# Kernel optimization log

Hardware: AMD Instinct MI355X
Metric: run time of the kernel (lower is better)

Reference implementation:

```python
import jax, jax.numpy as jnp
import numpy as np

N_NODES = 100000
N_EDGES = 3200000
D_FEAT = 128
HIDDEN = 16
N_CLASSES = 7


def gcn_conv(x, edge_index, edge_weight, W, b, n_nodes):
    h = x @ W  # dense projection first (Fout small)
    src, dst = edge_index[0], edge_index[1]
    # add self-loops with weight 1
    loop = jnp.arange(n_nodes, dtype=edge_index.dtype)
    src_a = jnp.concatenate([src, loop])
    dst_a = jnp.concatenate([dst, loop])
    ew_a = jnp.concatenate([edge_weight, jnp.ones((n_nodes,), dtype=x.dtype)])
    deg = jax.ops.segment_sum(ew_a, dst_a, num_segments=n_nodes)
    dinv = jnp.where(deg > 0, jax.lax.rsqrt(deg), 0.0)
    norm = dinv[src_a] * ew_a * dinv[dst_a]  # [E+N]
    msg = h[src_a] * norm[:, None]  # gather + scale
    out = jax.ops.segment_sum(msg, dst_a, num_segments=n_nodes)
    return out + b


def setup_inputs() -> dict:
    key = jax.random.key(0)
    k = jax.random.split(key, 8)
    x = jax.random.normal(k[0], (N_NODES, D_FEAT), dtype=jnp.float32)
    edge_index = jax.random.randint(k[1], (2, N_EDGES), 0, N_NODES, dtype=jnp.int64)
    edge_weight = jax.random.uniform(k[2], (N_EDGES,), dtype=jnp.float32)
    s1 = 1.0 / np.sqrt(D_FEAT)
    s2 = 1.0 / np.sqrt(HIDDEN)
    W1 = jax.random.uniform(k[3], (D_FEAT, HIDDEN), jnp.float32, -s1, s1)
    b1 = jnp.zeros((HIDDEN,), jnp.float32)
    W2 = jax.random.uniform(k[4], (HIDDEN, N_CLASSES), jnp.float32, -s2, s2)
    b2 = jnp.zeros((N_CLASSES,), jnp.float32)
    return {"x": x, "edge_index": edge_index, "edge_weight": edge_weight,
            "W1": W1, "b1": b1, "W2": W2, "b2": b2}


def reference(x, edge_index, edge_weight, W1, b1, W2, b2):
    h = jax.nn.relu(gcn_conv(x, edge_index, edge_weight, W1, b1, N_NODES))
    out = gcn_conv(h, edge_index, edge_weight, W2, b2, N_NODES)
    return jax.nn.log_softmax(out, axis=1)
```

## Files before the change

### kernel.cpp

```cpp
#include <hip/hip_runtime.h>
#include <hip/hip_fp16.h>
#include <math.h>

constexpr int NN = 100000;
constexpr int NE = 3200000;
constexpr int DF = 128;
constexpr int NH = 16;
constexpr int NC = 7;

constexpr int BN    = 256;
constexpr int NB    = (NN + BN - 1) / BN;
constexpr int CAP   = 9216;
constexpr int CHUNK = 4096;
constexpr int AB    = (NE + CHUNK - 1) / CHUNK;
constexpr int EPT   = CHUNK / 1024;
constexpr int SPT   = (CAP + 1023) / 1024;

constexpr float QS   = 32767.0f;
constexpr float QINV = 1.0f / 32767.0f;

typedef _Float16 half8 __attribute__((ext_vector_type(8)));
typedef float    f32x4 __attribute__((ext_vector_type(4)));

__global__ void k_zero(int* __restrict__ gcur) {
    int t = blockIdx.x * blockDim.x + threadIdx.x;
    if (t < NB) gcur[t] = 0;
}

__global__ void __launch_bounds__(1024)
k_append(const int* __restrict__ src,
         const int* __restrict__ dst,
         const float* __restrict__ w,
         int* __restrict__ gcur,
         uint2* __restrict__ ebuf) {
    __shared__ int hist[NB];
    __shared__ int cscan[512];
    __shared__ int basev[NB];
    __shared__ uint2 staged[CHUNK];
    __shared__ unsigned short sbkt[CHUNK];
    for (int i = threadIdx.x; i < NB; i += 1024) hist[i] = 0;
    __syncthreads();
    int e0 = blockIdx.x * CHUNK;
    unsigned slo[EPT], sw[EPT];
    int sbr[EPT];
#pragma unroll
    for (int k = 0; k < EPT; ++k) {
        int e = e0 + (int)threadIdx.x + k * 1024;
        sbr[k] = -1;
        if (e < NE) {
            int d = __builtin_nontemporal_load(dst + e);
            int b = d >> 8;
            int r = atomicAdd(&hist[b], 1);
            slo[k] = ((unsigned)(d & (BN - 1)) << 17) |
                     (unsigned)__builtin_nontemporal_load(src + e);
            sw[k]  = (unsigned)(__builtin_nontemporal_load(w + e) * QS + 0.5f);
            sbr[k] = (b << 13) | r;
        }
    }
    __syncthreads();
    {
        int v0 = (threadIdx.x < NB) ? hist[threadIdx.x] : 0;
        if (threadIdx.x < 512) cscan[threadIdx.x] = v0;
        __syncthreads();
        for (int off = 1; off < 512; off <<= 1) {
            int v = (threadIdx.x < 512 && threadIdx.x >= off) ? cscan[threadIdx.x - off] : 0;
            __syncthreads();
            if (threadIdx.x < 512) cscan[threadIdx.x] += v;
            __syncthreads();
        }
    }
    if (threadIdx.x < NB) {
        int c = hist[threadIdx.x];
        basev[threadIdx.x] = (c > 0) ? atomicAdd(&gcur[threadIdx.x], c) : 0;
    }
    __syncthreads();
#pragma unroll
    for (int k = 0; k < EPT; ++k) {
        if (sbr[k] >= 0) {
            int b = sbr[k] >> 13;
            int idx = (cscan[b] - hist[b]) + (sbr[k] & 0x1FFF);
            uint2 v; v.x = slo[k]; v.y = sw[k];
            staged[idx] = v;
            sbkt[idx] = (unsigned short)b;
        }
    }
    __syncthreads();
    int total = min(CHUNK, NE - e0);
    for (int i = threadIdx.x; i < total; i += 1024) {
        int b = sbkt[i];
        int st = cscan[b] - hist[b];
        int pos = basev[b] + (i - st);
        if (pos < CAP) ebuf[(size_t)b * CAP + pos] = staged[i];
    }
}

__global__ void __launch_bounds__(1024)
k_sort(const int* __restrict__ gcur,
       uint2* __restrict__ ebuf,
       int* __restrict__ rs,
       int* __restrict__ rc,
       float* __restrict__ dinv) {
    __shared__ int cursor[BN];
    __shared__ int scanS[BN];
    __shared__ int startEx[BN];
    __shared__ unsigned sorted[CAP];
    int b = blockIdx.x;
    int tid = threadIdx.x;
    int cnt = min(gcur[b], CAP);
    const uint2* eb = ebuf + (size_t)b * CAP;
    if (tid < BN) cursor[tid] = 0;
    __syncthreads();
    unsigned sval[SPT];
    int sdr[SPT];
#pragma unroll
    for (int k = 0; k < SPT; ++k) {
        int i = tid + k * 1024;
        sdr[k] = -1;
        if (i < cnt) {
            uint2 v = eb[i];
            int dl = (v.x >> 17) & (BN - 1);
            int r = atomicAdd(&cursor[dl], 1);
            sval[k] = (v.x & 0x1FFFF) | (v.y << 17);
            sdr[k] = (dl << 14) | r;
        }
    }
    __syncthreads();
    if (tid < BN) scanS[tid] = cursor[tid];
    __syncthreads();
    for (int off = 1; off < BN; off <<= 1) {
        int v = (tid < BN && tid >= off) ? scanS[tid - off] : 0;
        __syncthreads();
        if (tid < BN) scanS[tid] += v;
        __syncthreads();
    }
    if (tid < BN) {
        int ex = scanS[tid] - cursor[tid];
        startEx[tid] = ex;
        int n = b * BN + tid;
        if (n < NN) { rs[n] = b * CAP * 2 + ex; rc[n] = cursor[tid]; }
    }
    __syncthreads();
#pragma unroll
    for (int k = 0; k < SPT; ++k) {
        if (sdr[k] >= 0)
            sorted[startEx[sdr[k] >> 14] + (sdr[k] & 0x3FFF)] = sval[k];
    }
    __syncthreads();
    unsigned* eb32 = (unsigned*)ebuf + (size_t)b * CAP * 2;
    for (int i = tid; i < cnt; i += 1024) eb32[i] = sorted[i];
    {
        int node = tid >> 2, part = tid & 3;
        float s = (part == 0) ? 1.0f : 0.0f;
        int s0 = startEx[node], c = cursor[node];
        for (int i = part; i < c; i += 4) s += (float)(sorted[s0 + i] >> 17) * QINV;
        s += __shfl_xor(s, 1, 4);
        s += __shfl_xor(s, 2, 4);
        if (part == 0) {
            int n = b * BN + node;
            if (n < NN) dinv[n] = rsqrtf(s);
        }
    }
}

__global__ void __launch_bounds__(256)
k_proj1(const float* __restrict__ x,
        const float* __restrict__ W1,
        const float* __restrict__ dinv,
        __half* __restrict__ h1p) {
    int wave = threadIdx.x >> 6;
    int lane = threadIdx.x & 63;
    int tile = blockIdx.x * 4 + wave;
    if (tile * 16 >= NN) return;
    int m    = lane & 15;
    int quad = lane >> 4;
    half8 bfrag[4];
#pragma unroll
    for (int kc = 0; kc < 4; ++kc)
#pragma unroll
        for (int j = 0; j < 8; ++j)
            bfrag[kc][j] = (_Float16)W1[(kc * 32 + quad * 8 + j) * NH + m];
    int base = tile * 16;
    const float* xr = x + (size_t)(base + m) * DF + quad * 8;
    f32x4 acc = {0.f, 0.f, 0.f, 0.f};
#pragma unroll
    for (int kc = 0; kc < 4; ++kc) {
        const float4* p = (const float4*)(xr + kc * 32);
        float4 u0 = p[0];
        float4 u1 = p[1];
        half8 afrag;
        afrag[0] = (_Float16)u0.x; afrag[1] = (_Float16)u0.y;
        afrag[2] = (_Float16)u0.z; afrag[3] = (_Float16)u0.w;
        afrag[4] = (_Float16)u1.x; afrag[5] = (_Float16)u1.y;
        afrag[6] = (_Float16)u1.z; afrag[7] = (_Float16)u1.w;
        acc = __builtin_amdgcn_mfma_f32_16x16x32_f16(afrag, bfrag[kc], acc, 0, 0, 0);
    }
    float4 d4 = *(const float4*)(dinv + base + quad * 4);
#pragma unroll
    for (int reg = 0; reg < 4; ++reg) {
        float dd = (reg == 0) ? d4.x : (reg == 1) ? d4.y : (reg == 2) ? d4.z : d4.w;
        int row = quad * 4 + reg;
        h1p[(size_t)(base + row) * 16 + m] = __float2half(acc[reg] * dd);
    }
}

__global__ void __launch_bounds__(256)
k_agg1p(const int* __restrict__ rs,
        const int* __restrict__ rc,
        const unsigned* __restrict__ cbuf,
        const __half* __restrict__ h1p,
        const float* __restrict__ dinv,
        const float* __restrict__ b1,
        const float* __restrict__ W2,
        __half* __restrict__ h2p) {
    const uint2* hp4 = (const uint2*)h1p;
    int t = blockIdx.x * 256 + threadIdx.x;
    int n = t >> 2;
    int f4 = t & 3;
    if (n >= NN) return;
    float a0, a1, a2, a3;
    {
        uint2 u = hp4[n * 4 + f4];
        float2 lo = __half22float2(*(const __half2*)&u.x);
        float2 hi = __half22float2(*(const __half2*)&u.y);
        a0 = lo.x; a1 = lo.y; a2 = hi.x; a3 = hi.y;
    }
    int s0 = rs[n], c = rc[n];
    for (int i = 0; i < c; i += 8) {
        unsigned e[8];
        uint2 u[8];
#pragma unroll
        for (int k = 0; k < 8; ++k) {
            int idx = i + k;
            e[k] = (idx < c) ? __builtin_nontemporal_load(cbuf + s0 + idx) : 0u;
        }
#pragma unroll
        for (int k = 0; k < 8; ++k)
            u[k] = hp4[(e[k] & 0x1FFFF) * 4 + f4];
#pragma unroll
        for (int k = 0; k < 8; ++k) {
            float w = (float)(e[k] >> 17) * QINV;
            float2 lo = __half22float2(*(const __half2*)&u[k].x);
            float2 hi = __half22float2(*(const __half2*)&u[k].y);
            a0 += w * lo.x; a1 += w * lo.y; a2 += w * hi.x; a3 += w * hi.y;
        }
    }
    float di = dinv[n];
    int fb = 4 * f4;
    float hr0 = fmaxf(di * a0 + b1[fb + 0], 0.0f);
    float hr1 = fmaxf(di * a1 + b1[fb + 1], 0.0f);
    float hr2 = fmaxf(di * a2 + b1[fb + 2], 0.0f);
    float hr3 = fmaxf(di * a3 + b1[fb + 3], 0.0f);
    float p0, p1, p2, p3, p4, p5, p6;
    {
        const float* w0r = W2 + (fb + 0) * NC;
        const float* w1r = W2 + (fb + 1) * NC;
        const float* w2r = W2 + (fb + 2) * NC;
        const float* w3r = W2 + (fb + 3) * NC;
        p0 = hr0 * w0r[0] + hr1 * w1r[0] + hr2 * w2r[0] + hr3 * w3r[0];
        p1 = hr0 * w0r[1] + hr1 * w1r[1] + hr2 * w2r[1] + hr3 * w3r[1];
        p2 = hr0 * w0r[2] + hr1 * w1r[2] + hr2 * w2r[2] + hr3 * w3r[2];
        p3 = hr0 * w0r[3] + hr1 * w1r[3] + hr2 * w2r[3] + hr3 * w3r[3];
        p4 = hr0 * w0r[4] + hr1 * w1r[4] + hr2 * w2r[4] + hr3 * w3r[4];
        p5 = hr0 * w0r[5] + hr1 * w1r[5] + hr2 * w2r[5] + hr3 * w3r[5];
        p6 = hr0 * w0r[6] + hr1 * w1r[6] + hr2 * w2r[6] + hr3 * w3r[6];
    }
#pragma unroll
    for (int mask = 1; mask < 4; mask <<= 1) {
        p0 += __shfl_xor(p0, mask, 4);
        p1 += __shfl_xor(p1, mask, 4);
        p2 += __shfl_xor(p2, mask, 4);
        p3 += __shfl_xor(p3, mask, 4);
        p4 += __shfl_xor(p4, mask, 4);
        p5 += __shfl_xor(p5, mask, 4);
        p6 += __shfl_xor(p6, mask, 4);
    }
    float pa = (f4 == 0) ? p0 : (f4 == 1) ? p2 : (f4 == 2) ? p4 : p6;
    float pb = (f4 == 0) ? p1 : (f4 == 1) ? p3 : (f4 == 2) ? p5 : 0.0f;
    __half2 hv;
    hv.x = __float2half(di * pa);
    hv.y = __float2half(di * pb);
    ((__half2*)h2p)[n * 4 + f4] = hv;
}

__global__ void __launch_bounds__(256)
k_agg2_lsm(const int* __restrict__ rs,
           const int* __restrict__ rc,
           const unsigned* __restrict__ cbuf,
           const __half* __restrict__ h2p,
           const float* __restrict__ dinv,
           const float* __restrict__ b2,
           float* __restrict__ out) {
    const uint2* hp2 = (const uint2*)h2p;
    int t = blockIdx.x * 256 + threadIdx.x;
    int n = t >> 1;
    int c2 = t & 1;
    if (n >= NN) return;
    float a0, a1, a2, a3;
    {
        uint2 u = hp2[n * 2 + c2];
        float2 lo = __half22float2(*(const __half2*)&u.x);
        float2 hi = __half22float2(*(const __half2*)&u.y);
        a0 = lo.x; a1 = lo.y; a2 = hi.x; a3 = hi.y;
    }
    int s0 = rs[n], c = rc[n];
    for (int i = 0; i < c; i += 8) {
        unsigned e[8];
        uint2 u[8];
#pragma unroll
        for (int k = 0; k < 8; ++k) {
            int idx = i + k;
            e[k] = (idx < c) ? __builtin_nontemporal_load(cbuf + s0 + idx) : 0u;
        }
#pragma unroll
        for (int k = 0; k < 8; ++k)
            u[k] = hp2[(e[k] & 0x1FFFF) * 2 + c2];
#pragma unroll
        for (int k = 0; k < 8; ++k) {
            float w = (float)(e[k] >> 17) * QINV;
            float2 lo = __half22float2(*(const __half2*)&u[k].x);
            float2 hi = __half22float2(*(const __half2*)&u[k].y);
            a0 += w * lo.x; a1 += w * lo.y; a2 += w * hi.x; a3 += w * hi.y;
        }
    }
    float di = dinv[n];
    int cb = 4 * c2;
    float va0 = di * a0 + b2[cb + 0];
    float va1 = di * a1 + b2[cb + 1];
    float va2 = di * a2 + b2[cb + 2];
    float va3 = (c2 == 0) ? (di * a3 + b2[3]) : -1e30f;
    float m = fmaxf(fmaxf(va0, va1), fmaxf(va2, va3));
    m = fmaxf(m, __shfl_xor(m, 1, 2));
    float s = __expf(va0 - m) + __expf(va1 - m) + __expf(va2 - m) + __expf(va3 - m);
    s += __shfl_xor(s, 1, 2);
    float lse = m + __logf(s);
    int base = n * NC + cb;
    out[base + 0] = va0 - lse;
    out[base + 1] = va1 - lse;
    out[base + 2] = va2 - lse;
    if (c2 == 0) out[base + 3] = va3 - lse;
}

extern "C" void kernel_launch(void* const* d_in, const int* in_sizes, int n_in,
                              void* d_out, int out_size, void* d_ws, size_t ws_size,
                              hipStream_t stream) {
    const float* x  = (const float*)d_in[0];
    const int*   ei = (const int*)d_in[1];
    const float* ew = (const float*)d_in[2];
    const float* W1 = (const float*)d_in[3];
    const float* b1 = (const float*)d_in[4];
    const float* W2 = (const float*)d_in[5];
    const float* b2 = (const float*)d_in[6];
    float* out = (float*)d_out;

    const int* srcp = ei;
    const int* dstp = ei + NE;

    float*  ws   = (float*)d_ws;
    float*  dinv = ws;
    __half* h1p  = (__half*)(ws + 100352);
    __half* h2p  = (__half*)(ws + 900352);
    int*    gcur = (int*)(ws + 1300352);
    int*    rs   = (int*)(ws + 1301376);
    int*    rc   = (int*)(ws + 1401728);
    uint2*  ebuf = (uint2*)(ws + 1502080);
    const unsigned* cbuf = (const unsigned*)ebuf;

    auto cdiv = [](long long a, long long b) { return (int)((a + b - 1) / b); };

    k_zero<<<1, 1024, 0, stream>>>(gcur);
    k_append<<<AB, 1024, 0, stream>>>(srcp, dstp, ew, gcur, ebuf);
    k_sort<<<NB, 1024, 0, stream>>>(gcur, ebuf, rs, rc, dinv);
    k_proj1<<<cdiv(NN, 64), 256, 0, stream>>>(x, W1, dinv, h1p);
    k_agg1p<<<cdiv((long long)NN * 4, 256), 256, 0, stream>>>(rs, rc, cbuf, h1p, dinv, b1, W2, h2p);
    k_agg2_lsm<<<cdiv((long long)NN * 2, 256), 256, 0, stream>>>(rs, rc, cbuf, h2p, dinv, b2, out);
}
```

Before: 259.3 us.

## Replace per-node CSR sort with bucket-level aggregation via shared-memory atomics

Removes the per-bucket counting sort that built a CSR layout, and keeps edges only binned by 256-node destination bucket, with a separate byte array for the local destination. Degree and both aggregation layers now run one 1024-thread block per bucket, accumulating into padded shared-memory float arrays with LDS atomics. The append kernel's block scan is rewritten with wave shuffles, and the zero kernel is swapped for a memset. This trades the sort pass and its extra global traffic for heavy shared-atomic contention and per-edge 16-lane atomic fan-out. Float summation order also becomes nondeterministic.

```diff
diff --git a/kernel.cpp b/kernel.cpp
--- a/kernel.cpp
+++ b/kernel.cpp
@@ -14,64 +14,72 @@
 constexpr int CHUNK = 4096;
 constexpr int AB    = (NE + CHUNK - 1) / CHUNK;
 constexpr int EPT   = CHUNK / 1024;
-constexpr int SPT   = (CAP + 1023) / 1024;
 
 constexpr float QS   = 32767.0f;
 constexpr float QINV = 1.0f / 32767.0f;
 
 typedef _Float16 half8 __attribute__((ext_vector_type(8)));
 typedef float    f32x4 __attribute__((ext_vector_type(4)));
-
-__global__ void k_zero(int* __restrict__ gcur) {
-    int t = blockIdx.x * blockDim.x + threadIdx.x;
-    if (t < NB) gcur[t] = 0;
-}
 
 __global__ void __launch_bounds__(1024)
 k_append(const int* __restrict__ src,
          const int* __restrict__ dst,
          const float* __restrict__ w,
          int* __restrict__ gcur,
-         uint2* __restrict__ ebuf) {
+         unsigned* __restrict__ eval,
+         unsigned char* __restrict__ edl) {
     __shared__ int hist[NB];
     __shared__ int cscan[512];
     __shared__ int basev[NB];
-    __shared__ uint2 staged[CHUNK];
-    __shared__ unsigned short sbkt[CHUNK];
-    for (int i = threadIdx.x; i < NB; i += 1024) hist[i] = 0;
+    __shared__ int wsum[8];
+    __shared__ unsigned sval32[CHUNK];
+    __shared__ unsigned smeta[CHUNK];
+    int tid = threadIdx.x;
+    for (int i = tid; i < NB; i += 1024) hist[i] = 0;
     __syncthreads();
     int e0 = blockIdx.x * CHUNK;
-    unsigned slo[EPT], sw[EPT];
+    unsigned sv[EPT], sm[EPT];
     int sbr[EPT];
 #pragma unroll
     for (int k = 0; k < EPT; ++k) {
-        int e = e0 + (int)threadIdx.x + k * 1024;
+        int e = e0 + tid + k * 1024;
         sbr[k] = -1;
         if (e < NE) {
             int d = __builtin_nontemporal_load(dst + e);
             int b = d >> 8;
             int r = atomicAdd(&hist[b], 1);
-            slo[k] = ((unsigned)(d & (BN - 1)) << 17) |
-                     (unsigned)__builtin_nontemporal_load(src + e);
-            sw[k]  = (unsigned)(__builtin_nontemporal_load(w + e) * QS + 0.5f);
+            unsigned q = (unsigned)(__builtin_nontemporal_load(w + e) * QS + 0.5f);
+            sv[k] = (q << 17) |
+                    (unsigned)__builtin_nontemporal_load(src + e);
+            sm[k] = ((unsigned)b << 8) | (unsigned)(d & (BN - 1));
             sbr[k] = (b << 13) | r;
         }
     }
     __syncthreads();
     {
-        int v0 = (threadIdx.x < NB) ? hist[threadIdx.x] : 0;
-        if (threadIdx.x < 512) cscan[threadIdx.x] = v0;
+        int v = 0;
+        if (tid < 512) {
+            v = (tid < NB) ? hist[tid] : 0;
+#pragma unroll
+            for (int d = 1; d < 64; d <<= 1) {
+                int u = __shfl_up(v, d, 64);
+                if ((tid & 63) >= d) v += u;
+            }
+            if ((tid & 63) == 63) wsum[tid >> 6] = v;
+        }
         __syncthreads();
-        for (int off = 1; off < 512; off <<= 1) {
-            int v = (threadIdx.x < 512 && threadIdx.x >= off) ? cscan[threadIdx.x - off] : 0;
-            __syncthreads();
-            if (threadIdx.x < 512) cscan[threadIdx.x] += v;
-            __syncthreads();
-        }
-    }
-    if (threadIdx.x < NB) {
-        int c = hist[threadIdx.x];
-        basev[threadIdx.x] = (c > 0) ? atomicAdd(&gcur[threadIdx.x], c) : 0;
+        if (tid == 0) {
+            int acc = 0;
+#pragma unroll
+            for (int i = 0; i < 8; ++i) { int t = wsum[i]; wsum[i] = acc; acc += t; }
+        }
+        __syncthreads();
+        if (tid < 512) cscan[tid] = v + wsum[tid >> 6];
+    }
+    __syncthreads();
+    if (tid < NB) {
+        int c = hist[tid];
+        basev[tid] = (c > 0) ? atomicAdd(&gcur[tid], c) : 0;
     }
     __syncthreads();
 #pragma unroll
@@ -79,86 +87,46 @@
         if (sbr[k] >= 0) {
             int b = sbr[k] >> 13;
             int idx = (cscan[b] - hist[b]) + (sbr[k] & 0x1FFF);
-            uint2 v; v.x = slo[k]; v.y = sw[k];
-            staged[idx] = v;
-            sbkt[idx] = (unsigned short)b;
+            sval32[idx] = sv[k];
+            smeta[idx]  = sm[k];
         }
     }
     __syncthreads();
     int total = min(CHUNK, NE - e0);
-    for (int i = threadIdx.x; i < total; i += 1024) {
-        int b = sbkt[i];
+    for (int i = tid; i < total; i += 1024) {
+        unsigned mv = smeta[i];
+        int b = (int)(mv >> 8);
         int st = cscan[b] - hist[b];
         int pos = basev[b] + (i - st);
-        if (pos < CAP) ebuf[(size_t)b * CAP + pos] = staged[i];
+        if (pos < CAP) {
+            size_t g = (size_t)b * CAP + pos;
+            eval[g] = sval32[i];
+            edl[g]  = (unsigned char)(mv & 0xFF);
+        }
     }
 }
 
 __global__ void __launch_bounds__(1024)
-k_sort(const int* __restrict__ gcur,
-       uint2* __restrict__ ebuf,
-       int* __restrict__ rs,
-       int* __restrict__ rc,
+k_dinv(const int* __restrict__ gcur,
+       const unsigned* __restrict__ eval,
+       const unsigned char* __restrict__ edl,
        float* __restrict__ dinv) {
-    __shared__ int cursor[BN];
-    __shared__ int scanS[BN];
-    __shared__ int startEx[BN];
-    __shared__ unsigned sorted[CAP];
+    __shared__ float deg[BN];
     int b = blockIdx.x;
     int tid = threadIdx.x;
     int cnt = min(gcur[b], CAP);
-    const uint2* eb = ebuf + (size_t)b * CAP;
-    if (tid < BN) cursor[tid] = 0;
-    __syncthreads();
-    unsigned sval[SPT];
-    int sdr[SPT];
-#pragma unroll
-    for (int k = 0; k < SPT; ++k) {
-        int i = tid + k * 1024;
-        sdr[k] = -1;
-        if (i < cnt) {
-            uint2 v = eb[i];
-            int dl = (v.x >> 17) & (BN - 1);
-            int r = atomicAdd(&cursor[dl], 1);
-            sval[k] = (v.x & 0x1FFFF) | (v.y << 17);
-            sdr[k] = (dl << 14) | r;
-        }
-    }
-    __syncthreads();
-    if (tid < BN) scanS[tid] = cursor[tid];
-    __syncthreads();
-    for (int off = 1; off < BN; off <<= 1) {
-        int v = (tid < BN && tid >= off) ? scanS[tid - off] : 0;
-        __syncthreads();
-        if (tid < BN) scanS[tid] += v;
-        __syncthreads();
-    }
+    const unsigned* ev = eval + (size_t)b * CAP;
+    const unsigned char* ed = edl + (size_t)b * CAP;
+    if (tid < BN) deg[tid] = 1.0f;
+    __syncthreads();
+    for (int i = tid; i < cnt; i += 1024) {
+        float w = (float)(ev[i] >> 17) * QINV;
+        atomicAdd(&deg[ed[i]], w);
+    }
+    __syncthreads();
     if (tid < BN) {
-        int ex = scanS[tid] - cursor[tid];
-        startEx[tid] = ex;
         int n = b * BN + tid;
-        if (n < NN) { rs[n] = b * CAP * 2 + ex; rc[n] = cursor[tid]; }
-    }
-    __syncthreads();
-#pragma unroll
-    for (int k = 0; k < SPT; ++k) {
-        if (sdr[k] >= 0)
-            sorted[startEx[sdr[k] >> 14] + (sdr[k] & 0x3FFF)] = sval[k];
-    }
-    __syncthreads();
-    unsigned* eb32 = (unsigned*)ebuf + (size_t)b * CAP * 2;
-    for (int i = tid; i < cnt; i += 1024) eb32[i] = sorted[i];
-    {
-        int node = tid >> 2, part = tid & 3;
-        float s = (part == 0) ? 1.0f : 0.0f;
-        int s0 = startEx[node], c = cursor[node];
-        for (int i = part; i < c; i += 4) s += (float)(sorted[s0 + i] >> 17) * QINV;
-        s += __shfl_xor(s, 1, 4);
-        s += __shfl_xor(s, 2, 4);
-        if (part == 0) {
-            int n = b * BN + node;
-            if (n < NN) dinv[n] = rsqrtf(s);
-        }
+        if (n < NN) dinv[n] = rsqrtf(deg[tid]);
     }
 }
 
@@ -203,141 +171,158 @@
     }
 }
 
-__global__ void __launch_bounds__(256)
-k_agg1p(const int* __restrict__ rs,
-        const int* __restrict__ rc,
-        const unsigned* __restrict__ cbuf,
+__global__ void __launch_bounds__(1024)
+k_agg1B(const int* __restrict__ gcur,
+        const unsigned* __restrict__ eval,
+        const unsigned char* __restrict__ edl,
         const __half* __restrict__ h1p,
         const float* __restrict__ dinv,
         const float* __restrict__ b1,
         const float* __restrict__ W2,
         __half* __restrict__ h2p) {
-    const uint2* hp4 = (const uint2*)h1p;
-    int t = blockIdx.x * 256 + threadIdx.x;
-    int n = t >> 2;
-    int f4 = t & 3;
-    if (n >= NN) return;
-    float a0, a1, a2, a3;
+    __shared__ float accf[BN * 17];
+    int b = blockIdx.x;
+    int tid = threadIdx.x;
+    int cnt = min(gcur[b], CAP);
+    const unsigned* ev = eval + (size_t)b * CAP;
+    const unsigned char* ed = edl + (size_t)b * CAP;
+    for (int idx = tid; idx < BN * 16; idx += 1024) {
+        int node = idx >> 4, f = idx & 15;
+        int n = b * BN + node;
+        accf[node * 17 + f] = (n < NN) ? __half2float(h1p[(size_t)n * 16 + f]) : 0.0f;
+    }
+    __syncthreads();
+    for (int i = tid; i < cnt; i += 1024) {
+        unsigned e = ev[i];
+        int dl = (int)ed[i];
+        float w = (float)(e >> 17) * QINV;
+        const uint4* hp = (const uint4*)(h1p + (size_t)(e & 0x1FFFF) * 16);
+        uint4 ua = hp[0];
+        uint4 ub = hp[1];
+        float* ac = &accf[dl * 17];
+        float2 f0 = __half22float2(*(const __half2*)&ua.x);
+        float2 f1 = __half22float2(*(const __half2*)&ua.y);
+        float2 f2 = __half22float2(*(const __half2*)&ua.z);
+        float2 f3 = __half22float2(*(const __half2*)&ua.w);
+        float2 f4v = __half22float2(*(const __half2*)&ub.x);
+        float2 f5 = __half22float2(*(const __half2*)&ub.y);
+        float2 f6 = __half22float2(*(const __half2*)&ub.z);
+        float2 f7 = __half22float2(*(const __half2*)&ub.w);
+        atomicAdd(ac + 0,  w * f0.x);  atomicAdd(ac + 1,  w * f0.y);
+        atomicAdd(ac + 2,  w * f1.x);  atomicAdd(ac + 3,  w * f1.y);
+        atomicAdd(ac + 4,  w * f2.x);  atomicAdd(ac + 5,  w * f2.y);
+        atomicAdd(ac + 6,  w * f3.x);  atomicAdd(ac + 7,  w * f3.y);
+        atomicAdd(ac + 8,  w * f4v.x); atomicAdd(ac + 9,  w * f4v.y);
+        atomicAdd(ac + 10, w * f5.x);  atomicAdd(ac + 11, w * f5.y);
+        atomicAdd(ac + 12, w * f6.x);  atomicAdd(ac + 13, w * f6.y);
+        atomicAdd(ac + 14, w * f7.x);  atomicAdd(ac + 15, w * f7.y);
+    }
+    __syncthreads();
     {
-        uint2 u = hp4[n * 4 + f4];
-        float2 lo = __half22float2(*(const __half2*)&u.x);
-        float2 hi = __half22float2(*(const __half2*)&u.y);
-        a0 = lo.x; a1 = lo.y; a2 = hi.x; a3 = hi.y;
-    }
-    int s0 = rs[n], c = rc[n];
-    for (int i = 0; i < c; i += 8) {
-        unsigned e[8];
-        uint2 u[8];
-#pragma unroll
-        for (int k = 0; k < 8; ++k) {
-            int idx = i + k;
-            e[k] = (idx < c) ? __builtin_nontemporal_load(cbuf + s0 + idx) : 0u;
-        }
-#pragma unroll
-        for (int k = 0; k < 8; ++k)
-            u[k] = hp4[(e[k] & 0x1FFFF) * 4 + f4];
-#pragma unroll
-        for (int k = 0; k < 8; ++k) {
-            float w = (float)(e[k] >> 17) * QINV;
-            float2 lo = __half22float2(*(const __half2*)&u[k].x);
-            float2 hi = __half22float2(*(const __half2*)&u[k].y);
-            a0 += w * lo.x; a1 += w * lo.y; a2 += w * hi.x; a3 += w * hi.y;
-        }
-    }
-    float di = dinv[n];
-    int fb = 4 * f4;
-    float hr0 = fmaxf(di * a0 + b1[fb + 0], 0.0f);
-    float hr1 = fmaxf(di * a1 + b1[fb + 1], 0.0f);
-    float hr2 = fmaxf(di * a2 + b1[fb + 2], 0.0f);
-    float hr3 = fmaxf(di * a3 + b1[fb + 3], 0.0f);
-    float p0, p1, p2, p3, p4, p5, p6;
-    {
-        const float* w0r = W2 + (fb + 0) * NC;
-        const float* w1r = W2 + (fb + 1) * NC;
-        const float* w2r = W2 + (fb + 2) * NC;
-        const float* w3r = W2 + (fb + 3) * NC;
-        p0 = hr0 * w0r[0] + hr1 * w1r[0] + hr2 * w2r[0] + hr3 * w3r[0];
-        p1 = hr0 * w0r[1] + hr1 * w1r[1] + hr2 * w2r[1] + hr3 * w3r[1];
-        p2 = hr0 * w0r[2] + hr1 * w1r[2] + hr2 * w2r[2] + hr3 * w3r[2];
-        p3 = hr0 * w0r[3] + hr1 * w1r[3] + hr2 * w2r[3] + hr3 * w3r[3];
-        p4 = hr0 * w0r[4] + hr1 * w1r[4] + hr2 * w2r[4] + hr3 * w3r[4];
-        p5 = hr0 * w0r[5] + hr1 * w1r[5] + hr2 * w2r[5] + hr3 * w3r[5];
-        p6 = hr0 * w0r[6] + hr1 * w1r[6] + hr2 * w2r[6] + hr3 * w3r[6];
-    }
-#pragma unroll
-    for (int mask = 1; mask < 4; mask <<= 1) {
-        p0 += __shfl_xor(p0, mask, 4);
-        p1 += __shfl_xor(p1, mask, 4);
-        p2 += __shfl_xor(p2, mask, 4);
-        p3 += __shfl_xor(p3, mask, 4);
-        p4 += __shfl_xor(p4, mask, 4);
-        p5 += __shfl_xor(p5, mask, 4);
-        p6 += __shfl_xor(p6, mask, 4);
-    }
-    float pa = (f4 == 0) ? p0 : (f4 == 1) ? p2 : (f4 == 2) ? p4 : p6;
-    float pb = (f4 == 0) ? p1 : (f4 == 1) ? p3 : (f4 == 2) ? p5 : 0.0f;
-    __half2 hv;
-    hv.x = __float2half(di * pa);
-    hv.y = __float2half(di * pb);
-    ((__half2*)h2p)[n * 4 + f4] = hv;
-}
-
-__global__ void __launch_bounds__(256)
-k_agg2_lsm(const int* __restrict__ rs,
-           const int* __restrict__ rc,
-           const unsigned* __restrict__ cbuf,
-           const __half* __restrict__ h2p,
-           const float* __restrict__ dinv,
-           const float* __restrict__ b2,
-           float* __restrict__ out) {
-    const uint2* hp2 = (const uint2*)h2p;
-    int t = blockIdx.x * 256 + threadIdx.x;
-    int n = t >> 1;
-    int c2 = t & 1;
-    if (n >= NN) return;
-    float a0, a1, a2, a3;
-    {
-        uint2 u = hp2[n * 2 + c2];
-        float2 lo = __half22float2(*(const __half2*)&u.x);
-        float2 hi = __half22float2(*(const __half2*)&u.y);
-        a0 = lo.x; a1 = lo.y; a2 = hi.x; a3 = hi.y;
-    }
-    int s0 = rs[n], c = rc[n];
-    for (int i = 0; i < c; i += 8) {
-        unsigned e[8];
-        uint2 u[8];
-#pragma unroll
-        for (int k = 0; k < 8; ++k) {
-            int idx = i + k;
-            e[k] = (idx < c) ? __builtin_nontemporal_load(cbuf + s0 + idx) : 0u;
-        }
-#pragma unroll
-        for (int k = 0; k < 8; ++k)
-            u[k] = hp2[(e[k] & 0x1FFFF) * 2 + c2];
-#pragma unroll
-        for (int k = 0; k < 8; ++k) {
-            float w = (float)(e[k] >> 17) * QINV;
-            float2 lo = __half22float2(*(const __half2*)&u[k].x);
-            float2 hi = __half22float2(*(const __half2*)&u[k].y);
-            a0 += w * lo.x; a1 += w * lo.y; a2 += w * hi.x; a3 += w * hi.y;
-        }
-    }
-    float di = dinv[n];
-    int cb = 4 * c2;
-    float va0 = di * a0 + b2[cb + 0];
-    float va1 = di * a1 + b2[cb + 1];
-    float va2 = di * a2 + b2[cb + 2];
-    float va3 = (c2 == 0) ? (di * a3 + b2[3]) : -1e30f;
-    float m = fmaxf(fmaxf(va0, va1), fmaxf(va2, va3));
-    m = fmaxf(m, __shfl_xor(m, 1, 2));
-    float s = __expf(va0 - m) + __expf(va1 - m) + __expf(va2 - m) + __expf(va3 - m);
-    s += __shfl_xor(s, 1, 2);
-    float lse = m + __logf(s);
-    int base = n * NC + cb;
-    out[base + 0] = va0 - lse;
-    out[base + 1] = va1 - lse;
-    out[base + 2] = va2 - lse;
-    if (c2 == 0) out[base + 3] = va3 - lse;
+        int node = tid >> 2, f4 = tid & 3;
+        int n = b * BN + node;
+        if (n < NN) {
+            const float* ac = &accf[node * 17 + 4 * f4];
+            float di = dinv[n];
+            int fb = 4 * f4;
+            float hr0 = fmaxf(di * ac[0] + b1[fb + 0], 0.0f);
+            float hr1 = fmaxf(di * ac[1] + b1[fb + 1], 0.0f);
+            float hr2 = fmaxf(di * ac[2] + b1[fb + 2], 0.0f);
+            float hr3 = fmaxf(di * ac[3] + b1[fb + 3], 0.0f);
+            float p0, p1, p2, p3, p4, p5, p6;
+            {
+                const float* w0r = W2 + (fb + 0) * NC;
+                const float* w1r = W2 + (fb + 1) * NC;
+                const float* w2r = W2 + (fb + 2) * NC;
+                const float* w3r = W2 + (fb + 3) * NC;
+                p0 = hr0 * w0r[0] + hr1 * w1r[0] + hr2 * w2r[0] + hr3 * w3r[0];
+                p1 = hr0 * w0r[1] + hr1 * w1r[1] + hr2 * w2r[1] + hr3 * w3r[1];
+                p2 = hr0 * w0r[2] + hr1 * w1r[2] + hr2 * w2r[2] + hr3 * w3r[2];
+                p3 = hr0 * w0r[3] + hr1 * w1r[3] + hr2 * w2r[3] + hr3 * w3r[3];
+                p4 = hr0 * w0r[4] + hr1 * w1r[4] + hr2 * w2r[4] + hr3 * w3r[4];
+                p5 = hr0 * w0r[5] + hr1 * w1r[5] + hr2 * w2r[5] + hr3 * w3r[5];
+                p6 = hr0 * w0r[6] + hr1 * w1r[6] + hr2 * w2r[6] + hr3 * w3r[6];
+            }
+#pragma unroll
+            for (int mask = 1; mask < 4; mask <<= 1) {
+                p0 += __shfl_xor(p0, mask, 4);
+                p1 += __shfl_xor(p1, mask, 4);
+                p2 += __shfl_xor(p2, mask, 4);
+                p3 += __shfl_xor(p3, mask, 4);
+                p4 += __shfl_xor(p4, mask, 4);
+                p5 += __shfl_xor(p5, mask, 4);
+                p6 += __shfl_xor(p6, mask, 4);
+            }
+            float pa = (f4 == 0) ? p0 : (f4 == 1) ? p2 : (f4 == 2) ? p4 : p6;
+            float pb = (f4 == 0) ? p1 : (f4 == 1) ? p3 : (f4 == 2) ? p5 : 0.0f;
+            __half2 hv;
+            hv.x = __float2half(di * pa);
+            hv.y = __float2half(di * pb);
+            ((__half2*)h2p)[n * 4 + f4] = hv;
+        }
+    }
+}
+
+__global__ void __launch_bounds__(1024)
+k_agg2B(const int* __restrict__ gcur,
+        const unsigned* __restrict__ eval,
+        const unsigned char* __restrict__ edl,
+        const __half* __restrict__ h2p,
+        const float* __restrict__ dinv,
+        const float* __restrict__ b2,
+        float* __restrict__ out) {
+    __shared__ float acc2[BN * 9];
+    int b = blockIdx.x;
+    int tid = threadIdx.x;
+    int cnt = min(gcur[b], CAP);
+    const unsigned* ev = eval + (size_t)b * CAP;
+    const unsigned char* ed = edl + (size_t)b * CAP;
+    for (int idx = tid; idx < BN * 8; idx += 1024) {
+        int node = idx >> 3, f = idx & 7;
+        int n = b * BN + node;
+        acc2[node * 9 + f] = (n < NN) ? __half2float(h2p[(size_t)n * 8 + f]) : 0.0f;
+    }
+    __syncthreads();
+    for (int i = tid; i < cnt; i += 1024) {
+        unsigned e = ev[i];
+        int dl = (int)ed[i];
+        float w = (float)(e >> 17) * QINV;
+        uint4 u = *(const uint4*)(h2p + (size_t)(e & 0x1FFFF) * 8);
+        float* ac = &acc2[dl * 9];
+        float2 f0 = __half22float2(*(const __half2*)&u.x);
+        float2 f1 = __half22float2(*(const __half2*)&u.y);
+        float2 f2 = __half22float2(*(const __half2*)&u.z);
+        float2 f3 = __half22float2(*(const __half2*)&u.w);
+        atomicAdd(ac + 0, w * f0.x);  atomicAdd(ac + 1, w * f0.y);
+        atomicAdd(ac + 2, w * f1.x);  atomicAdd(ac + 3, w * f1.y);
+        atomicAdd(ac + 4, w * f2.x);  atomicAdd(ac + 5, w * f2.y);
+        atomicAdd(ac + 6, w * f3.x);
+    }
+    __syncthreads();
+    if (tid < BN * 2) {
+        int node = tid >> 1, c2 = tid & 1;
+        int n = b * BN + node;
+        if (n < NN) {
+            const float* ac = &acc2[node * 9 + 4 * c2];
+            float di = dinv[n];
+            int cb = 4 * c2;
+            float va0 = di * ac[0] + b2[cb + 0];
+            float va1 = di * ac[1] + b2[cb + 1];
+            float va2 = di * ac[2] + b2[cb + 2];
+            float va3 = (c2 == 0) ? (di * ac[3] + b2[3]) : -1e30f;
+            float m = fmaxf(fmaxf(va0, va1), fmaxf(va2, va3));
+            m = fmaxf(m, __shfl_xor(m, 1, 2));
+            float s = __expf(va0 - m) + __expf(va1 - m) + __expf(va2 - m)
+                    + ((c2 == 0) ? __expf(va3 - m) : 0.0f);
+            s += __shfl_xor(s, 1, 2);
+            float lse = m + __logf(s);
+            int base = n * NC + cb;
+            out[base + 0] = va0 - lse;
+            out[base + 1] = va1 - lse;
+            out[base + 2] = va2 - lse;
+            if (c2 == 0) out[base + 3] = va3 - lse;
+        }
+    }
 }
 
 extern "C" void kernel_launch(void* const* d_in, const int* in_sizes, int n_in,
@@ -360,17 +345,15 @@
     __half* h1p  = (__half*)(ws + 100352);
     __half* h2p  = (__half*)(ws + 900352);
     int*    gcur = (int*)(ws + 1300352);
-    int*    rs   = (int*)(ws + 1301376);
-    int*    rc   = (int*)(ws + 1401728);
-    uint2*  ebuf = (uint2*)(ws + 1502080);
-    const unsigned* cbuf = (const unsigned*)ebuf;
+    unsigned* eval = (unsigned*)(ws + 1301376);
+    unsigned char* edl = (unsigned char*)(ws + 4904832);
 
     auto cdiv = [](long long a, long long b) { return (int)((a + b - 1) / b); };
 
-    k_zero<<<1, 1024, 0, stream>>>(gcur);
-    k_append<<<AB, 1024, 0, stream>>>(srcp, dstp, ew, gcur, ebuf);
-    k_sort<<<NB, 1024, 0, stream>>>(gcur, ebuf, rs, rc, dinv);
+    hipMemsetAsync(gcur, 0, NB * sizeof(int), stream);
+    k_append<<<AB, 1024, 0, stream>>>(srcp, dstp, ew, gcur, eval, edl);
+    k_dinv<<<NB, 1024, 0, stream>>>(gcur, eval, edl, dinv);
     k_proj1<<<cdiv(NN, 64), 256, 0, stream>>>(x, W1, dinv, h1p);
-    k_agg1p<<<cdiv((long long)NN * 4, 256), 256, 0, stream>>>(rs, rc, cbuf, h1p, dinv, b1, W2, h2p);
-    k_agg2_lsm<<<cdiv((long long)NN * 2, 256), 256, 0, stream>>>(rs, rc, cbuf, h2p, dinv, b2, out);
-}
+    k_agg1B<<<NB, 1024, 0, stream>>>(gcur, eval, edl, h1p, dinv, b1, W2, h2p);
+    k_agg2B<<<NB, 1024, 0, stream>>>(gcur, eval, edl, h2p, dinv, b2, out);
+}
```

Result: slower. 667.9 us (+157.6%).
